# Performance work log

Measured on AMD Instinct MI355X. Metric: run time of the kernel, lower is better.

Reference implementation:

```python
import jax, jax.numpy as jnp
import numpy as np

B, T, C = 2, 2048, 1024
H, HD = 16, 64            # n_head, head_dim
R, ALPHA = 16, 32.0       # lora rank / alpha
KV_BITS = 8


def setup_inputs() -> dict:
    key = jax.random.key(0)
    ks = jax.random.split(key, 8)
    s = 0.02
    return {
        "hidden_states": jax.random.normal(ks[0], (B, T, C), jnp.float32),
        "W_attn": jax.random.normal(ks[1], (3 * C, C), jnp.float32) * s,
        "b_attn": jnp.zeros((3 * C,), jnp.float32),
        "A_attn": jax.random.normal(ks[2], (R, C), jnp.float32) * s,
        "B_attn": jnp.zeros((3 * C, R), jnp.float32),
        "W_proj": jax.random.normal(ks[3], (C, C), jnp.float32) * s,
        "b_proj": jnp.zeros((C,), jnp.float32),
        "A_proj": jax.random.normal(ks[4], (R, C), jnp.float32) * s,
        "B_proj": jnp.zeros((C, R), jnp.float32),
        "kv_scale": jnp.ones((1,), jnp.float32) * 0.05,
        "kv_zp": jnp.zeros((1,), jnp.float32),
    }


def lora_linear(x, W, b, A, Bm):
    # base linear + LoRA path (dropout identity in eval), scaling alpha/rank
    base = jnp.einsum('btc,oc->bto', x, W) + b
    lora = jnp.einsum('btr,or->bto', jnp.einsum('btc,rc->btr', x, A), Bm)
    return base + (ALPHA / R) * lora


def fake_quant(x, scale, zp):
    # learnable asymmetric fake-quantize with straight-through estimator
    qmax = float(2 ** KV_BITS - 1)
    q = jnp.clip(jnp.round(x / scale + zp), 0.0, qmax)
    deq = (q - zp) * scale
    return x + jax.lax.stop_gradient(deq - x)


def reference(hidden_states, W_attn, b_attn, A_attn, B_attn,
              W_proj, b_proj, A_proj, B_proj, kv_scale, kv_zp):
    qkv = lora_linear(hidden_states, W_attn, b_attn, A_attn, B_attn)  # [B,T,3C]
    q, k, v = jnp.split(qkv, 3, axis=2)
    # [B,H,T,HD]
    q = q.reshape(B, T, H, HD).transpose(0, 2, 1, 3)
    k = k.reshape(B, T, H, HD).transpose(0, 2, 1, 3)
    v = v.reshape(B, T, H, HD).transpose(0, 2, 1, 3)
    k = fake_quant(k, kv_scale, kv_zp)
    v = fake_quant(v, kv_scale, kv_zp)
    scores = jnp.einsum('bhqd,bhkd->bhqk', q, k) / np.sqrt(HD).astype(np.float32)
    causal = jnp.tril(jnp.ones((T, T), bool))
    scores = jnp.where(causal, scores, -jnp.inf)
    attn = jax.nn.softmax(scores, axis=-1)
    out = jnp.einsum('bhqk,bhkd->bhqd', attn, v)  # [B,H,T,HD]
    out = out.transpose(0, 2, 1, 3).reshape(B, T, C)
    return lora_linear(out, W_proj, b_proj, A_proj, B_proj)
```

## Files before the change

kernel.cpp:

```cpp
#include <hip/hip_runtime.h>
#include <math.h>

#define TT 2048
#define CDIM 1024
#define BT 4096
#define NT16 16

typedef __attribute__((ext_vector_type(8))) short bf16x8;
typedef __attribute__((ext_vector_type(4))) short short4v;
typedef __attribute__((ext_vector_type(4))) float f32x4;
typedef __attribute__((ext_vector_type(16))) float f32x16;

static __device__ __forceinline__ short f2bf(float f) {
  union { float f; unsigned int u; } c; c.f = f;
  unsigned int u = c.u;
  u += 0x7fff + ((u >> 16) & 1);
  return (short)(u >> 16);
}

static __device__ __forceinline__ void gload_lds16(const void* g, void* l) {
  __builtin_amdgcn_global_load_lds(
      (const __attribute__((address_space(1))) void*)g,
      (__attribute__((address_space(3))) void*)l, 16, 0, 0);
}

static __device__ __forceinline__ unsigned int cvt_pk_bf16(float lo, float hi) {
  unsigned int r;
  asm("v_cvt_pk_bf16_f32 %0, %1, %2" : "=v"(r) : "v"(lo), "v"(hi));
  return r;
}

__global__ __launch_bounds__(256) void packx_kernel(
    const float* __restrict__ x, short* __restrict__ Xb) {
  const size_t i = ((size_t)blockIdx.x * 256 + threadIdx.x) * 8;
  float4 v0 = *(const float4*)(x + i);
  float4 v1 = *(const float4*)(x + i + 4);
  bf16x8 p;
  p[0] = f2bf(v0.x); p[1] = f2bf(v0.y); p[2] = f2bf(v0.z); p[3] = f2bf(v0.w);
  p[4] = f2bf(v1.x); p[5] = f2bf(v1.y); p[6] = f2bf(v1.z); p[7] = f2bf(v1.w);
  *(bf16x8*)(Xb + i) = p;
}

__global__ __launch_bounds__(256) void packw_eff_kernel(
    const float* __restrict__ W, const float* __restrict__ Bm,
    const float* __restrict__ Aa, short* __restrict__ Waug) {
  __shared__ float Als[16 * 1024];
  const int tid = threadIdx.x;
  for (int i = tid; i < 4096; i += 256)
    ((float4*)Als)[i] = ((const float4*)Aa)[i];
  __syncthreads();
  const int row = blockIdx.x * 2 + (tid >> 7);
  const int c8 = (tid & 127) * 8;
  float4 w0 = *(const float4*)(W + (size_t)row * 1024 + c8);
  float4 w1 = *(const float4*)(W + (size_t)row * 1024 + c8 + 4);
  float acc[8] = {w0.x, w0.y, w0.z, w0.w, w1.x, w1.y, w1.z, w1.w};
  const float* brow = Bm + (size_t)row * 16;
#pragma unroll
  for (int r = 0; r < 16; r++) {
    float b2 = 2.f * brow[r];
#pragma unroll
    for (int j = 0; j < 8; j++) acc[j] += b2 * Als[r * 1024 + c8 + j];
  }
  bf16x8 p;
#pragma unroll
  for (int j = 0; j < 8; j++) p[j] = f2bf(acc[j]);
  *(bf16x8*)(Waug + (size_t)row * 1024 + c8) = p;
}

__global__ __launch_bounds__(512) void gemm256_qkv_kernel(
    const short* __restrict__ Amat, const short* __restrict__ Bmat,
    const float* __restrict__ bias,
    const float* __restrict__ kv_scale, const float* __restrict__ kv_zp,
    short* __restrict__ Qb, short* __restrict__ Kb, short* __restrict__ Vt) {
  __shared__ short lds[65536];
  char* const ldsB = (char*)lds;
  const int tid = threadIdx.x;
  const int lane = tid & 63;
  const int w = tid >> 6;
  const int wr = w >> 2, wc = w & 3;
  const int r16 = lane & 15, g = lane >> 4;

  const int x = blockIdx.x & 7;
  const int l = blockIdx.x >> 3;
  const int bm = ((x & 3) * 4 + (l & 3)) * 256;
  const int bn = ((x >> 2) * 6 + (l >> 2)) * 256;

  const int srow = tid >> 3;
  const int scg = (tid & 7) ^ (srow & 7);
  const int sdst = tid * 16;

#define STAGE_HALF(mat, rowbase, k0, ldsoff)                                  \
  do {                                                                        \
    const short* s_ = (mat) + (size_t)((rowbase) + srow) * CDIM + (k0) +      \
                      scg * 8;                                                \
    char* d_ = ldsB + (ldsoff) + sdst;                                        \
    gload_lds16(s_, d_);                                                      \
    gload_lds16(s_ + (size_t)64 * CDIM, d_ + 8192);                           \
  } while (0)

  f32x4 zero = {0.f, 0.f, 0.f, 0.f};
  f32x4 acc[8][4];
#pragma unroll
  for (int i = 0; i < 8; i++)
#pragma unroll
    for (int j = 0; j < 4; j++) acc[i][j] = zero;

  STAGE_HALF(Amat, bm, 0, 0);
  STAGE_HALF(Amat, bm + 128, 0, 16384);
  STAGE_HALF(Bmat, bn, 0, 32768);
  STAGE_HALF(Bmat, bn + 128, 0, 49152);

  const int bhalfbase = 32768 + (wc >> 1) * 16384;
  const int browbase = (wc & 1) * 64;

  for (int t = 0; t < NT16; ++t) {
    const int d = (t & 1) << 16;
    const int dn = ((t + 1) & 1) << 16;
    const int k1 = (t + 1) * 64;
    const bool st = (t < NT16 - 1);

    if (st) {
      STAGE_HALF(Amat, bm, k1, dn + 0);
      asm volatile("s_waitcnt vmcnt(2)" ::: "memory");
    } else {
      asm volatile("s_waitcnt vmcnt(0)" ::: "memory");
    }
    __builtin_amdgcn_s_barrier();
    __builtin_amdgcn_sched_barrier(0);

    bf16x8 breg[4][2];
#pragma unroll
    for (int ni = 0; ni < 4; ni++)
#pragma unroll
      for (int kk = 0; kk < 2; kk++) {
        int rowb = browbase + ni * 16 + r16;
        breg[ni][kk] = *(const bf16x8*)(
            ldsB + d + bhalfbase + rowb * 128 +
            (((kk * 4 + g) ^ (rowb & 7)) * 16));
      }
    {
      bf16x8 a0[2][2];
#pragma unroll
      for (int mi2 = 0; mi2 < 2; mi2++)
#pragma unroll
        for (int kk = 0; kk < 2; kk++) {
          int rowa = mi2 * 16 + r16;
          a0[mi2][kk] = *(const bf16x8*)(
              ldsB + d + wr * 16384 + rowa * 128 +
              (((kk * 4 + g) ^ (rowa & 7)) * 16));
        }
      asm volatile("s_waitcnt lgkmcnt(0)" ::: "memory");
      __builtin_amdgcn_sched_barrier(0);
      __builtin_amdgcn_s_setprio(1);
#pragma unroll
      for (int mi2 = 0; mi2 < 2; mi2++)
#pragma unroll
        for (int ni = 0; ni < 4; ni++)
#pragma unroll
          for (int kk = 0; kk < 2; kk++)
            acc[mi2][ni] = __builtin_amdgcn_mfma_f32_16x16x32_bf16(
                a0[mi2][kk], breg[ni][kk], acc[mi2][ni], 0, 0, 0);
      __builtin_amdgcn_s_setprio(0);
      __builtin_amdgcn_s_barrier();
    }

#pragma unroll
    for (int p = 1; p < 4; ++p) {
      bf16x8 ap[2][2];
#pragma unroll
      for (int mi2 = 0; mi2 < 2; mi2++)
#pragma unroll
        for (int kk = 0; kk < 2; kk++) {
          int rowa = (2 * p + mi2) * 16 + r16;
          ap[mi2][kk] = *(const bf16x8*)(
              ldsB + d + wr * 16384 + rowa * 128 +
              (((kk * 4 + g) ^ (rowa & 7)) * 16));
        }
      if (st) {
        if (p == 1)      STAGE_HALF(Amat, bm + 128, k1, dn + 16384);
        else if (p == 2) STAGE_HALF(Bmat, bn, k1, dn + 32768);
        else             STAGE_HALF(Bmat, bn + 128, k1, dn + 49152);
      }
      __builtin_amdgcn_s_barrier();
      asm volatile("s_waitcnt lgkmcnt(0)" ::: "memory");
      __builtin_amdgcn_sched_barrier(0);
      __builtin_amdgcn_s_setprio(1);
#pragma unroll
      for (int mi2 = 0; mi2 < 2; mi2++)
#pragma unroll
        for (int ni = 0; ni < 4; ni++)
#pragma unroll
          for (int kk = 0; kk < 2; kk++)
            acc[2 * p + mi2][ni] = __builtin_amdgcn_mfma_f32_16x16x32_bf16(
                ap[mi2][kk], breg[ni][kk], acc[2 * p + mi2][ni], 0, 0, 0);
      __builtin_amdgcn_s_setprio(0);
      __builtin_amdgcn_s_barrier();
    }
  }
#undef STAGE_HALF

  const float scale = kv_scale[0];
  const float zp = kv_zp[0];
  const int which = bn >> 10;
#pragma unroll
  for (int mi = 0; mi < 8; mi++)
#pragma unroll
    for (int ni = 0; ni < 4; ni++)
#pragma unroll
      for (int r = 0; r < 4; r++) {
        int m = bm + wr * 128 + mi * 16 + g * 4 + r;
        int n = bn + wc * 64 + ni * 16 + r16;
        float val = acc[mi][ni][r] + bias[n];
        int hn = n & 1023;
        int bhm = (m >> 11) * 16 + (hn >> 6);
        int tq = m & 2047;
        int dd = hn & 63;
        if (which == 0) {
          Qb[((size_t)bhm * TT + tq) * 64 + dd] =
              f2bf(val * 0.125f * 1.44269504088896340736f);
        } else {
          float q = rintf(val / scale + zp);
          q = fminf(fmaxf(q, 0.f), 255.f);
          float deq = (q - zp) * scale;
          if (which == 1) Kb[((size_t)bhm * TT + tq) * 64 + dd] = f2bf(deq);
          else            Vt[((size_t)bhm * 64 + dd) * TT + tq] = f2bf(deq);
        }
      }
}

__global__ __launch_bounds__(256) void gemm_proj_kernel(
    const short* __restrict__ Amat, const short* __restrict__ Bmat,
    const float* __restrict__ bias, float* __restrict__ Out) {
  __shared__ short lds[2 * 2 * 128 * 64];
  char* const ldsB = (char*)lds;
  const int tid = threadIdx.x;
  const int lane = tid & 63;
  const int wid = tid >> 6;
  const int wr = wid >> 1, wc = wid & 1;
  const int r16 = lane & 15, g = lane >> 4;

  const int x = blockIdx.x & 7;
  const int l = blockIdx.x >> 3;
  const int bm = ((x & 3) * 8 + (l & 7)) * 128;
  const int bn = (((x >> 2) * 4) + (l >> 3)) * 128;

#define STAGE_TILE(buf, k0)                                                   \
  do {                                                                        \
    _Pragma("unroll") for (int i = 0; i < 4; i++) {                           \
      int L = i * 256 + tid;                                                  \
      int row = L >> 3;                                                       \
      int cg = (L & 7) ^ (row & 7);                                           \
      char* d = ldsB + (buf) * 32768 + (i * 256 + wid * 64) * 16;             \
      gload_lds16(Amat + (size_t)(bm + row) * CDIM + (k0) + cg * 8, d);       \
      gload_lds16(Bmat + (size_t)(bn + row) * CDIM + (k0) + cg * 8,           \
                  d + 16384);                                                 \
    }                                                                         \
  } while (0)

  f32x4 zero = {0.f, 0.f, 0.f, 0.f};
  f32x4 acc[4][4];
#pragma unroll
  for (int i = 0; i < 4; i++)
#pragma unroll
    for (int j = 0; j < 4; j++) acc[i][j] = zero;

  STAGE_TILE(0, 0);
  asm volatile("s_waitcnt vmcnt(0)" ::: "memory");
  __builtin_amdgcn_s_barrier();
  __builtin_amdgcn_sched_barrier(0);

  int cur = 0;
  for (int t = 0; t < NT16; ++t) {
    if (t + 1 < NT16) STAGE_TILE(cur ^ 1, (t + 1) * 64);
    __builtin_amdgcn_sched_barrier(0);
    const char* Ab = ldsB + cur * 32768;
    const char* Bb = Ab + 16384;
#pragma unroll
    for (int kk = 0; kk < 2; kk++) {
      bf16x8 a[4], b[4];
#pragma unroll
      for (int mi = 0; mi < 4; mi++) {
        int row = wr * 64 + mi * 16 + r16;
        int cs = (kk * 4 + g) ^ (row & 7);
        a[mi] = *(const bf16x8*)(Ab + (row * 8 + cs) * 16);
      }
#pragma unroll
      for (int ni = 0; ni < 4; ni++) {
        int row = wc * 64 + ni * 16 + r16;
        int cs = (kk * 4 + g) ^ (row & 7);
        b[ni] = *(const bf16x8*)(Bb + (row * 8 + cs) * 16);
      }
      __builtin_amdgcn_s_setprio(1);
#pragma unroll
      for (int mi = 0; mi < 4; mi++)
#pragma unroll
        for (int ni = 0; ni < 4; ni++)
          acc[mi][ni] = __builtin_amdgcn_mfma_f32_16x16x32_bf16(
              a[mi], b[ni], acc[mi][ni], 0, 0, 0);
      __builtin_amdgcn_s_setprio(0);
    }
    asm volatile("s_waitcnt vmcnt(0)" ::: "memory");
    __builtin_amdgcn_s_barrier();
    __builtin_amdgcn_sched_barrier(0);
    cur ^= 1;
  }
#undef STAGE_TILE

#pragma unroll
  for (int mi = 0; mi < 4; mi++)
#pragma unroll
    for (int ni = 0; ni < 4; ni++)
#pragma unroll
      for (int r = 0; r < 4; r++) {
        int m = bm + wr * 64 + mi * 16 + g * 4 + r;
        int n = bn + wc * 64 + ni * 16 + r16;
        Out[(size_t)m * CDIM + n] = acc[mi][ni][r] + bias[n];
      }
}

__global__ __launch_bounds__(512) void attn_kernel(
    const short* __restrict__ Qb, const short* __restrict__ Kb,
    const short* __restrict__ Vt, short* __restrict__ Cb) {
  __shared__ short Kls[4 * 4096];
  __shared__ short Vls[4 * 4096];
  const int tid = threadIdx.x;
  const int lane = tid & 63;
  const int w = tid >> 6;
  const int qsub = w & 3;
  const int p = w >> 2;
  const int q32 = lane & 31;
  const int hi = lane >> 5;
  const int xid = blockIdx.x & 7;
  const int lix = blockIdx.x >> 3;
  const int bh = xid * 4 + (lix & 3);
  const int bx = lix >> 2;
  const size_t kvbase = (size_t)bh * TT * 64;
  const int swz = q32 & 7;
  const int b = bh >> 4, h = bh & 15;

  const int srow = tid >> 3;
  const int scg = (tid & 7) ^ (srow & 7);
  const int sdst = w * 1024;

  for (int seg = 0; seg < 2; seg++) {
    const int qb = seg ? bx : 15 - bx;
    const int q0 = qb * 128;
    const int q0w = q0 + qsub * 32;
    const int ns = qb + 1;

    bf16x8 qf[4];
    {
      const short* qp = Qb + kvbase + (size_t)(q0w + q32) * 64;
#pragma unroll
      for (int kd = 0; kd < 4; kd++)
        qf[kd] = *(const bf16x8*)(qp + kd * 16 + hi * 8);
    }
    f32x16 accT[2];
#pragma unroll
    for (int i = 0; i < 16; i++) { accT[0][i] = 0.f; accT[1][i] = 0.f; }
    float m_run = -1e30f, l_run = 0.f;

#pragma unroll
    for (int t2 = 0; t2 < 2; t2++) {
      int kv0 = t2 * 64;
      gload_lds16(Kb + kvbase + (size_t)(kv0 + srow) * 64 + scg * 8,
                  (char*)Kls + t2 * 8192 + sdst);
      gload_lds16(Vt + kvbase + (size_t)srow * TT + kv0 + scg * 8,
                  (char*)Vls + t2 * 8192 + sdst);
    }
    asm volatile("s_waitcnt vmcnt(0)" ::: "memory");
    __builtin_amdgcn_s_barrier();
    __builtin_amdgcn_sched_barrier(0);

    for (int s = 0; s < ns; s++) {
      if (s + 1 < ns) {
        const int bp = ((s + 1) & 1) * 2;
#pragma unroll
        for (int t2 = 0; t2 < 2; t2++) {
          int kv0 = (2 * (s + 1) + t2) * 64;
          gload_lds16(Kb + kvbase + (size_t)(kv0 + srow) * 64 + scg * 8,
                      (char*)Kls + (bp + t2) * 8192 + sdst);
          gload_lds16(Vt + kvbase + (size_t)srow * TT + kv0 + scg * 8,
                      (char*)Vls + (bp + t2) * 8192 + sdst);
        }
      }
      const int kv0 = (2 * s + p) * 64;
      if (kv0 <= q0w + 31) {
        const char* Kbase = (const char*)Kls + (2 * (s & 1) + p) * 8192;
        const char* Vbase = (const char*)Vls + (2 * (s & 1) + p) * 8192;
        f32x16 sA, sB;
#pragma unroll
        for (int i = 0; i < 16; i++) { sA[i] = 0.f; sB[i] = 0.f; }
        __builtin_amdgcn_s_setprio(1);
#pragma unroll
        for (int kd = 0; kd < 4; kd++) {
          int coff = ((kd * 2 + hi) ^ swz) * 16;
          bf16x8 a0 = *(const bf16x8*)(Kbase + q32 * 128 + coff);
          bf16x8 a1 = *(const bf16x8*)(Kbase + (32 + q32) * 128 + coff);
          sA = __builtin_amdgcn_mfma_f32_32x32x16_bf16(a0, qf[kd], sA, 0, 0, 0);
          sB = __builtin_amdgcn_mfma_f32_32x32x16_bf16(a1, qf[kd], sB, 0, 0, 0);
        }
        __builtin_amdgcn_s_setprio(0);
        const int qg = q0w + q32;
        if (kv0 + 63 > q0w) {
#pragma unroll
          for (int r = 0; r < 16; r++) {
            int kvr = kv0 + (r & 3) + 8 * (r >> 2) + 4 * hi;
            if (kvr > qg) sA[r] = -1e30f;
            if (kvr + 32 > qg) sB[r] = -1e30f;
          }
        }
        float mx = sA[0];
#pragma unroll
        for (int r = 1; r < 16; r++) mx = fmaxf(mx, sA[r]);
#pragma unroll
        for (int r = 0; r < 16; r++) mx = fmaxf(mx, sB[r]);
        mx = fmaxf(mx, __shfl_xor(mx, 32));
        float mnew = fmaxf(m_run, mx);
        float corr = exp2f(m_run - mnew);
        float rs = 0.f;
#pragma unroll
        for (int r = 0; r < 16; r++) {
          sA[r] = exp2f(sA[r] - mnew);
          sB[r] = exp2f(sB[r] - mnew);
          rs += sA[r] + sB[r];
        }
        rs += __shfl_xor(rs, 32);
        l_run = l_run * corr + rs;
        m_run = mnew;
#pragma unroll
        for (int r = 0; r < 16; r++) { accT[0][r] *= corr; accT[1][r] *= corr; }

        bf16x8 pf[4];
#pragma unroll
        for (int t2 = 0; t2 < 2; t2++) {
#pragma unroll
          for (int s01 = 0; s01 < 2; s01++) {
            int base = 8 * s01;
            unsigned int wlo0, wlo1, whi0, whi1;
            if (t2 == 0) {
              wlo0 = cvt_pk_bf16(sA[base + 0], sA[base + 1]);
              wlo1 = cvt_pk_bf16(sA[base + 2], sA[base + 3]);
              whi0 = cvt_pk_bf16(sA[base + 4], sA[base + 5]);
              whi1 = cvt_pk_bf16(sA[base + 6], sA[base + 7]);
            } else {
              wlo0 = cvt_pk_bf16(sB[base + 0], sB[base + 1]);
              wlo1 = cvt_pk_bf16(sB[base + 2], sB[base + 3]);
              whi0 = cvt_pk_bf16(sB[base + 4], sB[base + 5]);
              whi1 = cvt_pk_bf16(sB[base + 6], sB[base + 7]);
            }
            asm volatile("v_permlane32_swap_b32 %0, %1" : "+v"(wlo0), "+v"(whi0));
            asm volatile("v_permlane32_swap_b32 %0, %1" : "+v"(wlo1), "+v"(whi1));
            union { unsigned int u[4]; bf16x8 v; } cc;
            cc.u[0] = wlo0; cc.u[1] = wlo1; cc.u[2] = whi0; cc.u[3] = whi1;
            pf[t2 * 2 + s01] = cc.v;
          }
        }
        __builtin_amdgcn_s_setprio(1);
#pragma unroll
        for (int db = 0; db < 2; db++) {
          const int row = db * 32 + q32;
#pragma unroll
          for (int ks = 0; ks < 4; ks++) {
            bf16x8 vf = *(const bf16x8*)(Vbase + row * 128 +
                                         (((ks * 2 + hi) ^ swz) * 16));
            accT[db] = __builtin_amdgcn_mfma_f32_32x32x16_bf16(vf, pf[ks],
                                                               accT[db], 0, 0, 0);
          }
        }
        __builtin_amdgcn_s_setprio(0);
      }
      asm volatile("s_waitcnt vmcnt(0) lgkmcnt(0)" ::: "memory");
      __builtin_amdgcn_s_barrier();
      __builtin_amdgcn_sched_barrier(0);
    }

    float* scrO = (float*)Kls;
    float* scrML = (float*)Vls;
    if (p == 1) {
#pragma unroll
      for (int db = 0; db < 2; db++)
#pragma unroll
        for (int r = 0; r < 16; r++)
          scrO[qsub * 2048 + (db * 16 + r) * 64 + lane] = accT[db][r];
      scrML[qsub * 64 + lane] = m_run;
      scrML[256 + qsub * 64 + lane] = l_run;
    }
    __syncthreads();
    if (p == 0) {
      float m_o = scrML[qsub * 64 + lane];
      float l_o = scrML[256 + qsub * 64 + lane];
      float mm = fmaxf(m_run, m_o);
      float ce = exp2f(m_run - mm), co = exp2f(m_o - mm);
      float lt = l_run * ce + l_o * co;
      float rinv = 1.f / lt;
      short* cp = Cb + (size_t)(b * TT + q0w + q32) * CDIM + h * 64;
#pragma unroll
      for (int db = 0; db < 2; db++)
#pragma unroll
        for (int rg = 0; rg < 4; rg++) {
          short4v pk4;
#pragma unroll
          for (int rr = 0; rr < 4; rr++) {
            int r = rg * 4 + rr;
            float v = accT[db][r] * ce +
                      scrO[qsub * 2048 + (db * 16 + r) * 64 + lane] * co;
            pk4[rr] = f2bf(v * rinv);
          }
          *(short4v*)(cp + db * 32 + rg * 8 + hi * 4) = pk4;
        }
    }
    __syncthreads();
  }
}

extern "C" void kernel_launch(void* const* d_in, const int* in_sizes, int n_in,
                              void* d_out, int out_size, void* d_ws, size_t ws_size,
                              hipStream_t stream) {
  const float* x       = (const float*)d_in[0];
  const float* W_attn  = (const float*)d_in[1];
  const float* b_attn  = (const float*)d_in[2];
  const float* A_attn  = (const float*)d_in[3];
  const float* B_attn  = (const float*)d_in[4];
  const float* W_proj  = (const float*)d_in[5];
  const float* b_proj  = (const float*)d_in[6];
  const float* A_proj  = (const float*)d_in[7];
  const float* B_proj  = (const float*)d_in[8];
  const float* kv_scale = (const float*)d_in[9];
  const float* kv_zp    = (const float*)d_in[10];
  float* out = (float*)d_out;

  char* p = (char*)d_ws;
  short* Xb    = (short*)p; p += (size_t)BT * CDIM * 2;
  short* Waug1 = (short*)p; p += (size_t)3072 * CDIM * 2;
  short* Waug2 = (short*)p; p += (size_t)1024 * CDIM * 2;
  short* Cb    = (short*)p; p += (size_t)BT * CDIM * 2;
  short* Qb    = (short*)p; p += (size_t)32 * TT * 64 * 2;
  short* Kb    = (short*)p; p += (size_t)32 * TT * 64 * 2;
  short* Vt    = (short*)p; p += (size_t)32 * TT * 64 * 2;

  packx_kernel<<<dim3(2048), dim3(256), 0, stream>>>(x, Xb);
  packw_eff_kernel<<<dim3(1536), dim3(256), 0, stream>>>(
      W_attn, B_attn, A_attn, Waug1);
  packw_eff_kernel<<<dim3(512), dim3(256), 0, stream>>>(
      W_proj, B_proj, A_proj, Waug2);
  gemm256_qkv_kernel<<<dim3(192), dim3(512), 0, stream>>>(
      Xb, Waug1, b_attn, kv_scale, kv_zp, Qb, Kb, Vt);
  attn_kernel<<<dim3(256), dim3(512), 0, stream>>>(Qb, Kb, Vt, Cb);
  gemm_proj_kernel<<<dim3(256), dim3(256), 0, stream>>>(
      Cb, Waug2, b_proj, out);
}
```

Measured before the change: 147.5 us.

## Shrink QKV GEMM tile to 128x128 with 4 waves and quarter-staged prefetch

The QKV projection GEMM moves from 256x256 tiles with 512 threads (192 blocks) to 128x128 tiles with 256 threads (768 blocks). Next-k staging is split into four A/B quarter loads interleaved between the four MFMA sub-steps, with fewer barriers per iteration. The goal is better fill of the 256 CUs, which the 192-block grid left partly idle, and smaller LDS use per block so more blocks can be resident. The cost is lower operand reuse per tile, so more global and LDS traffic per FLOP.

```diff
diff --git a/kernel.cpp b/kernel.cpp
--- a/kernel.cpp
+++ b/kernel.cpp
@@ -67,63 +67,60 @@
   *(bf16x8*)(Waug + (size_t)row * 1024 + c8) = p;
 }
 
-__global__ __launch_bounds__(512) void gemm256_qkv_kernel(
+__global__ __launch_bounds__(256) void gemm_qkv_kernel(
     const short* __restrict__ Amat, const short* __restrict__ Bmat,
     const float* __restrict__ bias,
     const float* __restrict__ kv_scale, const float* __restrict__ kv_zp,
     short* __restrict__ Qb, short* __restrict__ Kb, short* __restrict__ Vt) {
-  __shared__ short lds[65536];
+  __shared__ short lds[2 * 2 * 128 * 64];
   char* const ldsB = (char*)lds;
   const int tid = threadIdx.x;
   const int lane = tid & 63;
-  const int w = tid >> 6;
-  const int wr = w >> 2, wc = w & 3;
+  const int wid = tid >> 6;
+  const int wr = wid >> 1, wc = wid & 1;
   const int r16 = lane & 15, g = lane >> 4;
 
   const int x = blockIdx.x & 7;
   const int l = blockIdx.x >> 3;
-  const int bm = ((x & 3) * 4 + (l & 3)) * 256;
-  const int bn = ((x >> 2) * 6 + (l >> 2)) * 256;
-
-  const int srow = tid >> 3;
-  const int scg = (tid & 7) ^ (srow & 7);
-  const int sdst = tid * 16;
-
-#define STAGE_HALF(mat, rowbase, k0, ldsoff)                                  \
+  const int bm = ((x & 3) * 8 + (l & 7)) * 128;
+  const int bn = (((x >> 2) * 12) + (l >> 3)) * 128;
+
+#define STAGE_U(mat, rowbase, k0, i, buf, off)                                \
   do {                                                                        \
-    const short* s_ = (mat) + (size_t)((rowbase) + srow) * CDIM + (k0) +      \
-                      scg * 8;                                                \
-    char* d_ = ldsB + (ldsoff) + sdst;                                        \
-    gload_lds16(s_, d_);                                                      \
-    gload_lds16(s_ + (size_t)64 * CDIM, d_ + 8192);                           \
+    int L_ = (i) * 256 + tid;                                                 \
+    int row_ = L_ >> 3;                                                       \
+    int cg_ = (L_ & 7) ^ (row_ & 7);                                          \
+    gload_lds16((mat) + (size_t)((rowbase) + row_) * CDIM + (k0) + cg_ * 8,   \
+                ldsB + (buf) * 32768 + (off) + (i) * 4096 + wid * 1024);      \
   } while (0)
+#define STAGE_A(i, buf, k0) STAGE_U(Amat, bm, k0, i, buf, 0)
+#define STAGE_B(i, buf, k0) STAGE_U(Bmat, bn, k0, i, buf, 16384)
 
   f32x4 zero = {0.f, 0.f, 0.f, 0.f};
-  f32x4 acc[8][4];
-#pragma unroll
-  for (int i = 0; i < 8; i++)
+  f32x4 acc[4][4];
+#pragma unroll
+  for (int i = 0; i < 4; i++)
 #pragma unroll
     for (int j = 0; j < 4; j++) acc[i][j] = zero;
 
-  STAGE_HALF(Amat, bm, 0, 0);
-  STAGE_HALF(Amat, bm + 128, 0, 16384);
-  STAGE_HALF(Bmat, bn, 0, 32768);
-  STAGE_HALF(Bmat, bn + 128, 0, 49152);
-
-  const int bhalfbase = 32768 + (wc >> 1) * 16384;
-  const int browbase = (wc & 1) * 64;
+  STAGE_A(0, 0, 0); STAGE_A(2, 0, 0);
+  STAGE_B(0, 0, 0); STAGE_B(2, 0, 0);
+  STAGE_B(1, 0, 0); STAGE_B(3, 0, 0);
+  STAGE_A(1, 0, 0); STAGE_A(3, 0, 0);
 
   for (int t = 0; t < NT16; ++t) {
-    const int d = (t & 1) << 16;
-    const int dn = ((t + 1) & 1) << 16;
+    const int cur = t & 1;
+    const int nxt = cur ^ 1;
     const int k1 = (t + 1) * 64;
-    const bool st = (t < NT16 - 1);
+    const bool st = (t + 1 < NT16);
+    const char* Ab = ldsB + cur * 32768;
+    const char* Bb = Ab + 16384;
 
     if (st) {
-      STAGE_HALF(Amat, bm, k1, dn + 0);
+      STAGE_A(0, nxt, k1); STAGE_A(2, nxt, k1);
+      asm volatile("s_waitcnt vmcnt(4)" ::: "memory");
+    } else {
       asm volatile("s_waitcnt vmcnt(2)" ::: "memory");
-    } else {
-      asm volatile("s_waitcnt vmcnt(0)" ::: "memory");
     }
     __builtin_amdgcn_s_barrier();
     __builtin_amdgcn_sched_barrier(0);
@@ -133,82 +130,114 @@
     for (int ni = 0; ni < 4; ni++)
 #pragma unroll
       for (int kk = 0; kk < 2; kk++) {
-        int rowb = browbase + ni * 16 + r16;
-        breg[ni][kk] = *(const bf16x8*)(
-            ldsB + d + bhalfbase + rowb * 128 +
-            (((kk * 4 + g) ^ (rowb & 7)) * 16));
+        int row = wc * 64 + ni * 16 + r16;
+        int cs = (kk * 4 + g) ^ (row & 7);
+        breg[ni][kk] = *(const bf16x8*)(Bb + (row * 8 + cs) * 16);
       }
     {
-      bf16x8 a0[2][2];
-#pragma unroll
-      for (int mi2 = 0; mi2 < 2; mi2++)
-#pragma unroll
-        for (int kk = 0; kk < 2; kk++) {
-          int rowa = mi2 * 16 + r16;
-          a0[mi2][kk] = *(const bf16x8*)(
-              ldsB + d + wr * 16384 + rowa * 128 +
-              (((kk * 4 + g) ^ (rowa & 7)) * 16));
-        }
+      bf16x8 a0[2];
+#pragma unroll
+      for (int kk = 0; kk < 2; kk++) {
+        int row = wr * 64 + r16;
+        int cs = (kk * 4 + g) ^ (row & 7);
+        a0[kk] = *(const bf16x8*)(Ab + (row * 8 + cs) * 16);
+      }
       asm volatile("s_waitcnt lgkmcnt(0)" ::: "memory");
       __builtin_amdgcn_sched_barrier(0);
       __builtin_amdgcn_s_setprio(1);
 #pragma unroll
-      for (int mi2 = 0; mi2 < 2; mi2++)
-#pragma unroll
-        for (int ni = 0; ni < 4; ni++)
-#pragma unroll
-          for (int kk = 0; kk < 2; kk++)
-            acc[mi2][ni] = __builtin_amdgcn_mfma_f32_16x16x32_bf16(
-                a0[mi2][kk], breg[ni][kk], acc[mi2][ni], 0, 0, 0);
+      for (int ni = 0; ni < 4; ni++)
+#pragma unroll
+        for (int kk = 0; kk < 2; kk++)
+          acc[0][ni] = __builtin_amdgcn_mfma_f32_16x16x32_bf16(
+              a0[kk], breg[ni][kk], acc[0][ni], 0, 0, 0);
       __builtin_amdgcn_s_setprio(0);
-      __builtin_amdgcn_s_barrier();
-    }
-
-#pragma unroll
-    for (int p = 1; p < 4; ++p) {
-      bf16x8 ap[2][2];
-#pragma unroll
-      for (int mi2 = 0; mi2 < 2; mi2++)
-#pragma unroll
-        for (int kk = 0; kk < 2; kk++) {
-          int rowa = (2 * p + mi2) * 16 + r16;
-          ap[mi2][kk] = *(const bf16x8*)(
-              ldsB + d + wr * 16384 + rowa * 128 +
-              (((kk * 4 + g) ^ (rowa & 7)) * 16));
-        }
-      if (st) {
-        if (p == 1)      STAGE_HALF(Amat, bm + 128, k1, dn + 16384);
-        else if (p == 2) STAGE_HALF(Bmat, bn, k1, dn + 32768);
-        else             STAGE_HALF(Bmat, bn + 128, k1, dn + 49152);
-      }
-      __builtin_amdgcn_s_barrier();
+    }
+
+    if (st) { STAGE_B(0, nxt, k1); STAGE_B(2, nxt, k1); }
+    {
+      bf16x8 a1[2];
+#pragma unroll
+      for (int kk = 0; kk < 2; kk++) {
+        int row = wr * 64 + 16 + r16;
+        int cs = (kk * 4 + g) ^ (row & 7);
+        a1[kk] = *(const bf16x8*)(Ab + (row * 8 + cs) * 16);
+      }
       asm volatile("s_waitcnt lgkmcnt(0)" ::: "memory");
       __builtin_amdgcn_sched_barrier(0);
       __builtin_amdgcn_s_setprio(1);
 #pragma unroll
-      for (int mi2 = 0; mi2 < 2; mi2++)
-#pragma unroll
-        for (int ni = 0; ni < 4; ni++)
-#pragma unroll
-          for (int kk = 0; kk < 2; kk++)
-            acc[2 * p + mi2][ni] = __builtin_amdgcn_mfma_f32_16x16x32_bf16(
-                ap[mi2][kk], breg[ni][kk], acc[2 * p + mi2][ni], 0, 0, 0);
+      for (int ni = 0; ni < 4; ni++)
+#pragma unroll
+        for (int kk = 0; kk < 2; kk++)
+          acc[1][ni] = __builtin_amdgcn_mfma_f32_16x16x32_bf16(
+              a1[kk], breg[ni][kk], acc[1][ni], 0, 0, 0);
       __builtin_amdgcn_s_setprio(0);
-      __builtin_amdgcn_s_barrier();
+    }
+
+    if (st) {
+      STAGE_B(1, nxt, k1); STAGE_B(3, nxt, k1);
+      asm volatile("s_waitcnt vmcnt(6)" ::: "memory");
+    } else {
+      asm volatile("s_waitcnt vmcnt(0)" ::: "memory");
+    }
+    __builtin_amdgcn_s_barrier();
+    __builtin_amdgcn_sched_barrier(0);
+    {
+      bf16x8 a2[2];
+#pragma unroll
+      for (int kk = 0; kk < 2; kk++) {
+        int row = wr * 64 + 32 + r16;
+        int cs = (kk * 4 + g) ^ (row & 7);
+        a2[kk] = *(const bf16x8*)(Ab + (row * 8 + cs) * 16);
+      }
+      asm volatile("s_waitcnt lgkmcnt(0)" ::: "memory");
+      __builtin_amdgcn_sched_barrier(0);
+      __builtin_amdgcn_s_setprio(1);
+#pragma unroll
+      for (int ni = 0; ni < 4; ni++)
+#pragma unroll
+        for (int kk = 0; kk < 2; kk++)
+          acc[2][ni] = __builtin_amdgcn_mfma_f32_16x16x32_bf16(
+              a2[kk], breg[ni][kk], acc[2][ni], 0, 0, 0);
+      __builtin_amdgcn_s_setprio(0);
+    }
+
+    if (st) { STAGE_A(1, nxt, k1); STAGE_A(3, nxt, k1); }
+    {
+      bf16x8 a3[2];
+#pragma unroll
+      for (int kk = 0; kk < 2; kk++) {
+        int row = wr * 64 + 48 + r16;
+        int cs = (kk * 4 + g) ^ (row & 7);
+        a3[kk] = *(const bf16x8*)(Ab + (row * 8 + cs) * 16);
+      }
+      asm volatile("s_waitcnt lgkmcnt(0)" ::: "memory");
+      __builtin_amdgcn_sched_barrier(0);
+      __builtin_amdgcn_s_setprio(1);
+#pragma unroll
+      for (int ni = 0; ni < 4; ni++)
+#pragma unroll
+        for (int kk = 0; kk < 2; kk++)
+          acc[3][ni] = __builtin_amdgcn_mfma_f32_16x16x32_bf16(
+              a3[kk], breg[ni][kk], acc[3][ni], 0, 0, 0);
+      __builtin_amdgcn_s_setprio(0);
     }
   }
-#undef STAGE_HALF
+#undef STAGE_A
+#undef STAGE_B
+#undef STAGE_U
 
   const float scale = kv_scale[0];
   const float zp = kv_zp[0];
   const int which = bn >> 10;
 #pragma unroll
-  for (int mi = 0; mi < 8; mi++)
+  for (int mi = 0; mi < 4; mi++)
 #pragma unroll
     for (int ni = 0; ni < 4; ni++)
 #pragma unroll
       for (int r = 0; r < 4; r++) {
-        int m = bm + wr * 128 + mi * 16 + g * 4 + r;
+        int m = bm + wr * 64 + mi * 16 + g * 4 + r;
         int n = bn + wc * 64 + ni * 16 + r16;
         float val = acc[mi][ni][r] + bias[n];
         int hn = n & 1023;
@@ -544,7 +573,7 @@
       W_attn, B_attn, A_attn, Waug1);
   packw_eff_kernel<<<dim3(512), dim3(256), 0, stream>>>(
       W_proj, B_proj, A_proj, Waug2);
-  gemm256_qkv_kernel<<<dim3(192), dim3(512), 0, stream>>>(
+  gemm_qkv_kernel<<<dim3(768), dim3(256), 0, stream>>>(
       Xb, Waug1, b_attn, kv_scale, kv_zp, Qb, Kb, Vt);
   attn_kernel<<<dim3(256), dim3(512), 0, stream>>>(Qb, Kb, Vt, Cb);
   gemm_proj_kernel<<<dim3(256), dim3(256), 0, stream>>>(
```

Result: faster. 134.8 us (-8.6%).

## Simplify QKV GEMM pipeline to whole-tile double buffering with one barrier per step

Applied to the files above, without the earlier changes.

Replaces the QKV GEMM's finely interleaved four-phase schedule, which issued staging loads per quarter and used several barriers per k-step, with a plain double-buffered loop. The loop prefetches the whole next 256x256x64 tile at the start of each step, computes on the current buffer in two k-halves, then waits and does a single barrier. It also adds a min-blocks hint of 2 to launch_bounds, which caps register use. The aim is fewer barriers and a simpler schedule, at the cost of less fine-grained overlap and possible register spills under the tighter bound. The 128 KiB LDS footprint likely still limits occupancy to one block per CU.

```diff
diff --git a/kernel.cpp b/kernel.cpp
--- a/kernel.cpp
+++ b/kernel.cpp
@@ -67,7 +67,7 @@
   *(bf16x8*)(Waug + (size_t)row * 1024 + c8) = p;
 }
 
-__global__ __launch_bounds__(512) void gemm256_qkv_kernel(
+__global__ __launch_bounds__(512, 2) void gemm_qkv_kernel(
     const short* __restrict__ Amat, const short* __restrict__ Bmat,
     const float* __restrict__ bias,
     const float* __restrict__ kv_scale, const float* __restrict__ kv_zp,
@@ -85,17 +85,17 @@
   const int bm = ((x & 3) * 4 + (l & 3)) * 256;
   const int bn = ((x >> 2) * 6 + (l >> 2)) * 256;
 
-  const int srow = tid >> 3;
-  const int scg = (tid & 7) ^ (srow & 7);
-  const int sdst = tid * 16;
-
-#define STAGE_HALF(mat, rowbase, k0, ldsoff)                                  \
+#define STAGE_TILE(buf, k0)                                                   \
   do {                                                                        \
-    const short* s_ = (mat) + (size_t)((rowbase) + srow) * CDIM + (k0) +      \
-                      scg * 8;                                                \
-    char* d_ = ldsB + (ldsoff) + sdst;                                        \
-    gload_lds16(s_, d_);                                                      \
-    gload_lds16(s_ + (size_t)64 * CDIM, d_ + 8192);                           \
+    _Pragma("unroll") for (int i = 0; i < 4; i++) {                           \
+      int L = i * 512 + tid;                                                  \
+      int row = L >> 3;                                                       \
+      int cg = (L & 7) ^ (row & 7);                                           \
+      char* d = ldsB + (buf) * 65536 + L * 16;                                \
+      gload_lds16(Amat + (size_t)(bm + row) * CDIM + (k0) + cg * 8, d);       \
+      gload_lds16(Bmat + (size_t)(bn + row) * CDIM + (k0) + cg * 8,           \
+                  d + 32768);                                                 \
+    }                                                                         \
   } while (0)
 
   f32x4 zero = {0.f, 0.f, 0.f, 0.f};
@@ -105,99 +105,51 @@
 #pragma unroll
     for (int j = 0; j < 4; j++) acc[i][j] = zero;
 
-  STAGE_HALF(Amat, bm, 0, 0);
-  STAGE_HALF(Amat, bm + 128, 0, 16384);
-  STAGE_HALF(Bmat, bn, 0, 32768);
-  STAGE_HALF(Bmat, bn + 128, 0, 49152);
-
-  const int bhalfbase = 32768 + (wc >> 1) * 16384;
-  const int browbase = (wc & 1) * 64;
-
+  STAGE_TILE(0, 0);
+  asm volatile("s_waitcnt vmcnt(0)" ::: "memory");
+  __builtin_amdgcn_s_barrier();
+  __builtin_amdgcn_sched_barrier(0);
+
+  int cur = 0;
   for (int t = 0; t < NT16; ++t) {
-    const int d = (t & 1) << 16;
-    const int dn = ((t + 1) & 1) << 16;
-    const int k1 = (t + 1) * 64;
-    const bool st = (t < NT16 - 1);
-
-    if (st) {
-      STAGE_HALF(Amat, bm, k1, dn + 0);
-      asm volatile("s_waitcnt vmcnt(2)" ::: "memory");
-    } else {
-      asm volatile("s_waitcnt vmcnt(0)" ::: "memory");
-    }
+    if (t + 1 < NT16) STAGE_TILE(cur ^ 1, (t + 1) * 64);
+    __builtin_amdgcn_sched_barrier(0);
+    const char* Ab = ldsB + cur * 65536;
+    const char* Bb = Ab + 32768;
+#pragma unroll
+    for (int kk = 0; kk < 2; kk++) {
+      bf16x8 b[4];
+#pragma unroll
+      for (int ni = 0; ni < 4; ni++) {
+        int row = wc * 64 + ni * 16 + r16;
+        int cs = (kk * 4 + g) ^ (row & 7);
+        b[ni] = *(const bf16x8*)(Bb + (row * 8 + cs) * 16);
+      }
+#pragma unroll
+      for (int mh = 0; mh < 2; mh++) {
+        bf16x8 a[4];
+#pragma unroll
+        for (int mi = 0; mi < 4; mi++) {
+          int row = wr * 128 + (mh * 4 + mi) * 16 + r16;
+          int cs = (kk * 4 + g) ^ (row & 7);
+          a[mi] = *(const bf16x8*)(Ab + (row * 8 + cs) * 16);
+        }
+        __builtin_amdgcn_s_setprio(1);
+#pragma unroll
+        for (int mi = 0; mi < 4; mi++)
+#pragma unroll
+          for (int ni = 0; ni < 4; ni++)
+            acc[mh * 4 + mi][ni] = __builtin_amdgcn_mfma_f32_16x16x32_bf16(
+                a[mi], b[ni], acc[mh * 4 + mi][ni], 0, 0, 0);
+        __builtin_amdgcn_s_setprio(0);
+      }
+    }
+    asm volatile("s_waitcnt vmcnt(0)" ::: "memory");
     __builtin_amdgcn_s_barrier();
     __builtin_amdgcn_sched_barrier(0);
-
-    bf16x8 breg[4][2];
-#pragma unroll
-    for (int ni = 0; ni < 4; ni++)
-#pragma unroll
-      for (int kk = 0; kk < 2; kk++) {
-        int rowb = browbase + ni * 16 + r16;
-        breg[ni][kk] = *(const bf16x8*)(
-            ldsB + d + bhalfbase + rowb * 128 +
-            (((kk * 4 + g) ^ (rowb & 7)) * 16));
-      }
-    {
-      bf16x8 a0[2][2];
-#pragma unroll
-      for (int mi2 = 0; mi2 < 2; mi2++)
-#pragma unroll
-        for (int kk = 0; kk < 2; kk++) {
-          int rowa = mi2 * 16 + r16;
-          a0[mi2][kk] = *(const bf16x8*)(
-              ldsB + d + wr * 16384 + rowa * 128 +
-              (((kk * 4 + g) ^ (rowa & 7)) * 16));
-        }
-      asm volatile("s_waitcnt lgkmcnt(0)" ::: "memory");
-      __builtin_amdgcn_sched_barrier(0);
-      __builtin_amdgcn_s_setprio(1);
-#pragma unroll
-      for (int mi2 = 0; mi2 < 2; mi2++)
-#pragma unroll
-        for (int ni = 0; ni < 4; ni++)
-#pragma unroll
-          for (int kk = 0; kk < 2; kk++)
-            acc[mi2][ni] = __builtin_amdgcn_mfma_f32_16x16x32_bf16(
-                a0[mi2][kk], breg[ni][kk], acc[mi2][ni], 0, 0, 0);
-      __builtin_amdgcn_s_setprio(0);
-      __builtin_amdgcn_s_barrier();
-    }
-
-#pragma unroll
-    for (int p = 1; p < 4; ++p) {
-      bf16x8 ap[2][2];
-#pragma unroll
-      for (int mi2 = 0; mi2 < 2; mi2++)
-#pragma unroll
-        for (int kk = 0; kk < 2; kk++) {
-          int rowa = (2 * p + mi2) * 16 + r16;
-          ap[mi2][kk] = *(const bf16x8*)(
-              ldsB + d + wr * 16384 + rowa * 128 +
-              (((kk * 4 + g) ^ (rowa & 7)) * 16));
-        }
-      if (st) {
-        if (p == 1)      STAGE_HALF(Amat, bm + 128, k1, dn + 16384);
-        else if (p == 2) STAGE_HALF(Bmat, bn, k1, dn + 32768);
-        else             STAGE_HALF(Bmat, bn + 128, k1, dn + 49152);
-      }
-      __builtin_amdgcn_s_barrier();
-      asm volatile("s_waitcnt lgkmcnt(0)" ::: "memory");
-      __builtin_amdgcn_sched_barrier(0);
-      __builtin_amdgcn_s_setprio(1);
-#pragma unroll
-      for (int mi2 = 0; mi2 < 2; mi2++)
-#pragma unroll
-        for (int ni = 0; ni < 4; ni++)
-#pragma unroll
-          for (int kk = 0; kk < 2; kk++)
-            acc[2 * p + mi2][ni] = __builtin_amdgcn_mfma_f32_16x16x32_bf16(
-                ap[mi2][kk], breg[ni][kk], acc[2 * p + mi2][ni], 0, 0, 0);
-      __builtin_amdgcn_s_setprio(0);
-      __builtin_amdgcn_s_barrier();
-    }
+    cur ^= 1;
   }
-#undef STAGE_HALF
+#undef STAGE_TILE
 
   const float scale = kv_scale[0];
   const float zp = kv_zp[0];
@@ -544,7 +496,7 @@
       W_attn, B_attn, A_attn, Waug1);
   packw_eff_kernel<<<dim3(512), dim3(256), 0, stream>>>(
       W_proj, B_proj, A_proj, Waug2);
-  gemm256_qkv_kernel<<<dim3(192), dim3(512), 0, stream>>>(
+  gemm_qkv_kernel<<<dim3(192), dim3(512), 0, stream>>>(
       Xb, Waug1, b_attn, kv_scale, kv_zp, Qb, Kb, Vt);
   attn_kernel<<<dim3(256), dim3(512), 0, stream>>>(Qb, Kb, Vt, Cb);
   gemm_proj_kernel<<<dim3(256), dim3(256), 0, stream>>>(
```

After: 146.8 us. Within noise of the previous version (-0.5%).
